# Performance work log

Hardware: AMD Instinct MI355X
Metric: run time of the kernel (lower is better)

The kernel has to match this reference:

```python
import jax, jax.numpy as jnp
import numpy as np

R = 64  # all tensor-ring ranks equal

def setup_inputs() -> dict:
    key = jax.random.key(0)
    k1, k2, k3 = jax.random.split(key, 3)
    B, T, N, M, C = 512, 64, 512, 64, 100
    # xavier-uniform-ish scale for weights (gain=init_value=1.0)
    s_sh = float(np.sqrt(6.0 / (R * N + R)))
    s_la = float(np.sqrt(6.0 / (C * R * M + R)))
    return {
        "tensor": jax.random.normal(k1, (B, T, N), dtype=jnp.float32),
        "W_shared": jax.random.uniform(k2, (R, N, R), dtype=jnp.float32, minval=-s_sh, maxval=s_sh),
        "W_last": jax.random.uniform(k3, (C, R, M, R), dtype=jnp.float32, minval=-s_la, maxval=s_la),
    }

def reference(tensor, W_shared, W_last):
    B = tensor.shape[0]
    xt = jnp.transpose(tensor, (1, 0, 2))  # [T, B, N]
    state0 = jnp.ones((R, B, R), dtype=tensor.dtype)  # [r1, B, r2]
    # per-step: x = einsum('bj,rbi->rbji'); state = einsum('ijk,rbji->rbk')
    # == einsum('bj,rbi,ijk->rbk'); factored to avoid the [r,b,n,r] intermediate
    def step(state, x_t):
        bik = jnp.einsum('bj,ijk->bik', x_t, W_shared)   # [B, r2, r3]
        new = jnp.einsum('rbi,bik->rbk', state, bik)     # [r1, B, r3]
        return new, None
    state, _ = jax.lax.scan(step, state0, xt)
    # last kernel with pad_input = ones(B, m):
    # einsum('cijk,rbji->cbrk') with x[r,b,j,i]=state[r,b,i] == sum over j of W_last
    W_sum = jnp.sum(W_last, axis=2)                      # [C, r2, r_last]
    state = jnp.einsum('cik,rbi->cbrk', W_sum, state)    # [C, B, r1, r_last]
    # trace over the last two (square) rank dims
    out = jnp.einsum('cbrr->cb', state)                  # [C, B]
    return out
```

## Files before the change

### kernel.cpp

```cpp
#include <hip/hip_runtime.h>
#include <hip/hip_fp16.h>


typedef _Float16 f16;
typedef __attribute__((ext_vector_type(8))) _Float16 f16x8;
typedef __attribute__((ext_vector_type(2))) _Float16 f16x2;
typedef __attribute__((ext_vector_type(4))) float f32x4;

#define GLDS16(g, l)                                                      \
    __builtin_amdgcn_global_load_lds(                                     \
        (const __attribute__((address_space(1))) void*)(g),               \
        (__attribute__((address_space(3))) void*)(l), 16, 0, 0)

#define BARRIER() asm volatile("s_barrier" ::: "memory")
#define VMCNT(n) asm volatile("s_waitcnt vmcnt(" #n ")" ::: "memory")

__global__ __launch_bounds__(256) void k_usum(const float* __restrict__ Wl,
                                              float* __restrict__ u) {
    int ci = blockIdx.x;
    const float4* p = (const float4*)(Wl + (size_t)ci * 4096);
    int tid = threadIdx.x;
    float s = 0.f;
#pragma unroll
    for (int q = 0; q < 4; ++q) {
        float4 v = p[tid + 256 * q];
        s += v.x + v.y + v.z + v.w;
    }
    __shared__ float red[256];
    red[tid] = s;
    __syncthreads();
    if (tid < 128) red[tid] += red[tid + 128];
    __syncthreads();
    if (tid < 64) {
        float x = red[tid] + red[tid + 64];
#pragma unroll
        for (int off = 32; off > 0; off >>= 1) x += __shfl_down(x, off, 64);
        if (tid == 0) u[ci] = x;
    }
}

__global__ __launch_bounds__(256) void k_cvtA(const float* __restrict__ in,
                                              f16* __restrict__ out) {
    int idx = blockIdx.x * 256 + threadIdx.x;
    const float4* p = (const float4*)in + (size_t)idx * 2;
    float4 v0 = p[0], v1 = p[1];
    f16x8 h;
    h[0] = (f16)v0.x; h[1] = (f16)v0.y; h[2] = (f16)v0.z; h[3] = (f16)v0.w;
    h[4] = (f16)v1.x; h[5] = (f16)v1.y; h[6] = (f16)v1.z; h[7] = (f16)v1.w;
    *(f16x8*)(out + (size_t)idx * 8) = h;
}

__global__ __launch_bounds__(256) void k_cvtW(const float* __restrict__ W,
                                              f16* __restrict__ Bt) {
    int o = blockIdx.x * 256 + threadIdx.x;
    int col = o >> 8;
    int j = (o & 255) << 1;
    int i = col >> 6, k = col & 63;
    const float* src = W + ((size_t)i * 512 + j) * 64 + k;
    f16x2 pk;
    pk[0] = (f16)src[0];
    pk[1] = (f16)src[64];
    *(f16x2*)(Bt + (size_t)col * 512 + j) = pk;
}


#define STAGE_A(qq, ha, ktv) do {                                             \
    _Pragma("unroll") for (int u_ = 0; u_ < 2; ++u_) {                        \
        int idx_ = (wid * 2 + u_) * 64 + lane;                                \
        int r_ = idx_ >> 3;                                                   \
        int ls_ = (idx_ & 7) ^ (r_ & 7);                                      \
        const f16* g_ = A + (size_t)(m0 + (ha) * 128 + r_) * 512              \
                          + (ktv) * 64 + ls_ * 8;                             \
        char* l_ = smem + (qq) * 65536 + (ha) * 16384 + (wid * 2 + u_) * 1024;\
        GLDS16(g_, l_);                                                       \
    } } while (0)

#define STAGE_B(qq, hb, ktv) do {                                             \
    _Pragma("unroll") for (int u_ = 0; u_ < 2; ++u_) {                        \
        int idx_ = (wid * 2 + u_) * 64 + lane;                                \
        int r_ = idx_ >> 3;                                                   \
        int ls_ = (idx_ & 7) ^ (r_ & 7);                                      \
        const f16* g_ = Bt + (size_t)(n0 + (hb) * 128 + r_) * 512             \
                           + (ktv) * 64 + ls_ * 8;                            \
        char* l_ = smem + (qq) * 65536 + 32768 + (hb) * 16384                 \
                        + (wid * 2 + u_) * 1024;                              \
        GLDS16(g_, l_);                                                       \
    } } while (0)

#define RD_A(ha, ktv) do {                                                    \
    _Pragma("unroll") for (int mf_ = 0; mf_ < 4; ++mf_)                       \
    _Pragma("unroll") for (int kq_ = 0; kq_ < 2; ++kq_) {                     \
        int ra_ = wr * 64 + mf_ * 16 + (lane & 15);                           \
        int off_ = ((ra_ << 7) + kq_ * 64 + ((lane >> 4) << 4))               \
                   ^ ((ra_ & 7) << 4);                                        \
        a[mf_][kq_] = *(const f16x8*)(smem + ((ktv) & 1) * 65536              \
                                      + (ha) * 16384 + off_);                 \
    } } while (0)

#define RD_B(hb, ktv, breg) do {                                              \
    _Pragma("unroll") for (int nf_ = 0; nf_ < 2; ++nf_)                       \
    _Pragma("unroll") for (int kq_ = 0; kq_ < 2; ++kq_) {                     \
        int rb_ = wc * 32 + nf_ * 16 + (lane & 15);                           \
        int off_ = ((rb_ << 7) + kq_ * 64 + ((lane >> 4) << 4))               \
                   ^ ((rb_ & 7) << 4);                                        \
        breg[nf_][kq_] = *(const f16x8*)(smem + ((ktv) & 1) * 65536           \
                                         + 32768 + (hb) * 16384 + off_);      \
    } } while (0)

#define MFMA_Q(qa_, qb_, breg) do {                                           \
    __builtin_amdgcn_s_setprio(1);                                            \
    _Pragma("unroll") for (int mf_ = 0; mf_ < 4; ++mf_)                       \
    _Pragma("unroll") for (int nf_ = 0; nf_ < 2; ++nf_)                       \
    _Pragma("unroll") for (int kq_ = 0; kq_ < 2; ++kq_)                       \
        acc[qa_][qb_][mf_][nf_] = __builtin_amdgcn_mfma_f32_16x16x32_f16(     \
            a[mf_][kq_], breg[nf_][kq_], acc[qa_][qb_][mf_][nf_], 0, 0, 0);   \
    __builtin_amdgcn_s_setprio(0);                                            \
    } while (0)

__global__ __launch_bounds__(512) void k_gemm_256(const f16* __restrict__ A,
                                                  const f16* __restrict__ Bt,
                                                  __half* __restrict__ outp) {
    extern __shared__ char smem[];
    const int tid = threadIdx.x;
    const int lane = tid & 63;
    const int wid = tid >> 6;
    int lin = blockIdx.x;
    int swz = (lin & 7) * 256 + (lin >> 3);
    const int n0 = (swz & 15) * 256;
    const int m0 = (swz >> 4) * 256;
    const int wr = wid >> 2, wc = wid & 3;

    f32x4 acc[2][2][4][2];
#pragma unroll
    for (int x = 0; x < 2; ++x)
#pragma unroll
        for (int y = 0; y < 2; ++y)
#pragma unroll
            for (int z = 0; z < 4; ++z)
#pragma unroll
                for (int w = 0; w < 2; ++w) acc[x][y][z][w] = (f32x4)0.f;

    f16x8 a[4][2], b0[2][2], b1[2][2];

    STAGE_A(0, 0, 0);
    STAGE_B(0, 0, 0);
    STAGE_B(0, 1, 0);
    STAGE_A(0, 1, 0);
    STAGE_A(1, 0, 1);
    STAGE_B(1, 0, 1);
    STAGE_B(1, 1, 1);

    for (int kt = 0; kt < 6; ++kt) {
        VMCNT(6);
        BARRIER();
        RD_A(0, kt);
        RD_B(0, kt, b0);
        STAGE_A((kt + 1) & 1, 1, kt + 1);
        MFMA_Q(0, 0, b0);
        BARRIER();
        RD_B(1, kt, b1);
        MFMA_Q(0, 1, b1);
        BARRIER();
        RD_A(1, kt);
        STAGE_A(kt & 1, 0, kt + 2);
        STAGE_B(kt & 1, 0, kt + 2);
        MFMA_Q(1, 0, b0);
        BARRIER();
        STAGE_B(kt & 1, 1, kt + 2);
        MFMA_Q(1, 1, b1);
        BARRIER();
    }
    {
        VMCNT(6);
        BARRIER();
        RD_A(0, 6);
        RD_B(0, 6, b0);
        STAGE_A(1, 1, 7);
        MFMA_Q(0, 0, b0);
        BARRIER();
        RD_B(1, 6, b1);
        MFMA_Q(0, 1, b1);
        BARRIER();
        RD_A(1, 6);
        MFMA_Q(1, 0, b0);
        BARRIER();
        MFMA_Q(1, 1, b1);
        BARRIER();
    }
    {
        VMCNT(0);
        BARRIER();
        RD_A(0, 7);
        RD_B(0, 7, b0);
        MFMA_Q(0, 0, b0);
        BARRIER();
        RD_B(1, 7, b1);
        MFMA_Q(0, 1, b1);
        BARRIER();
        RD_A(1, 7);
        MFMA_Q(1, 0, b0);
        BARRIER();
        MFMA_Q(1, 1, b1);
        BARRIER();
    }

    __half* Cs = (__half*)smem;
#pragma unroll
    for (int qa = 0; qa < 2; ++qa)
#pragma unroll
        for (int qb = 0; qb < 2; ++qb)
#pragma unroll
            for (int mf = 0; mf < 4; ++mf)
#pragma unroll
                for (int nf = 0; nf < 2; ++nf)
#pragma unroll
                    for (int j = 0; j < 4; ++j) {
                        int row = qa * 128 + wr * 64 + mf * 16 + ((lane >> 4) << 2) + j;
                        int col = qb * 128 + wc * 32 + nf * 16 + (lane & 15);
                        Cs[row * 256 + col] = __float2half(acc[qa][qb][mf][nf][j]);
                    }
    BARRIER();
#pragma unroll
    for (int it = 0; it < 16; ++it) {
        int idx = it * 512 + tid;
        int r = idx >> 5, seg = idx & 31;
        *(float4*)(outp + (size_t)(m0 + r) * 4096 + n0 + seg * 8) =
            *(const float4*)(Cs + r * 256 + seg * 8);
    }
}

#define BM 128
#define BN 64
#define BK 32
__global__ __launch_bounds__(256) void k_gemm(const float* __restrict__ A,
                                              const float* __restrict__ W,
                                              __half* __restrict__ out,
                                              int a_off, int a_stride) {
    __shared__ float As[BK * BM];
    __shared__ float Bs[BK * BN];
    int i0 = blockIdx.x;
    int m0 = blockIdx.y * BM;
    int tid = threadIdx.x;
    int tx = tid & 15, ty = tid >> 4;
    float acc[8][4];
#pragma unroll
    for (int q = 0; q < 8; ++q)
#pragma unroll
        for (int c = 0; c < 4; ++c) acc[q][c] = 0.f;
    const float* wbase = W + (size_t)i0 * 32768;
    for (int j0 = 0; j0 < 512; j0 += BK) {
        {
            int c4 = tid & 7;
            int r = tid >> 3;
#pragma unroll
            for (int p = 0; p < 4; ++p) {
                int row = r + 32 * p;
                float4 v = *(const float4*)(A + (size_t)a_off +
                                            (size_t)(m0 + row) * a_stride + j0 + 4 * c4);
                As[(4 * c4 + 0) * BM + row] = v.x;
                As[(4 * c4 + 1) * BM + row] = v.y;
                As[(4 * c4 + 2) * BM + row] = v.z;
                As[(4 * c4 + 3) * BM + row] = v.w;
            }
            const float4* src = (const float4*)(wbase + (size_t)j0 * 64);
            float4* dst = (float4*)Bs;
            dst[tid] = src[tid];
            dst[tid + 256] = src[tid + 256];
        }
        __syncthreads();
#pragma unroll
        for (int kk = 0; kk < BK; ++kk) {
            float bv[4], av[8];
#pragma unroll
            for (int c = 0; c < 4; ++c) bv[c] = Bs[kk * BN + 4 * tx + c];
#pragma unroll
            for (int q = 0; q < 8; ++q) av[q] = As[kk * BM + 8 * ty + q];
#pragma unroll
            for (int q = 0; q < 8; ++q)
#pragma unroll
                for (int c = 0; c < 4; ++c) acc[q][c] += av[q] * bv[c];
        }
        __syncthreads();
    }
#pragma unroll
    for (int q = 0; q < 8; ++q) {
        int m = m0 + 8 * ty + q;
        __half* o = out + (size_t)m * 4096 + i0 * 64 + 4 * tx;
#pragma unroll
        for (int c = 0; c < 4; ++c) o[c] = __float2half(acc[q][c]);
    }
}

__global__ __launch_bounds__(256) void k_scan(const __half* __restrict__ bik,
                                              const float* __restrict__ u,
                                              float* __restrict__ out) {
    int b = blockIdx.x;
    int tid = threadIdx.x;
    int k = tid & 63, grp = tid >> 6;
    __shared__ float vsh[64];
    __shared__ float part[256];
    if (tid < 64) vsh[tid] = 1.0f;
    const __half* base = bik + (size_t)b * 64 * 4096 + grp * 16 * 64 + k;
    __half bufA[16], bufB[16];
#pragma unroll
    for (int q = 0; q < 16; ++q) bufA[q] = base[q * 64];
    __syncthreads();
    for (int t = 0; t < 64; t += 2) {
        {
            const __half* pn = base + (size_t)(t + 1) * 4096;
#pragma unroll
            for (int q = 0; q < 16; ++q) bufB[q] = pn[q * 64];
            float s = 0.f;
#pragma unroll
            for (int q = 0; q < 16; ++q) s += vsh[grp * 16 + q] * __half2float(bufA[q]);
            part[tid] = s;
            __syncthreads();
            if (tid < 64) vsh[k] = part[k] + part[64 + k] + part[128 + k] + part[192 + k];
            __syncthreads();
        }
        {
            int t2 = (t + 2 < 64) ? (t + 2) : 63;
            const __half* pn = base + (size_t)t2 * 4096;
#pragma unroll
            for (int q = 0; q < 16; ++q) bufA[q] = pn[q * 64];
            float s = 0.f;
#pragma unroll
            for (int q = 0; q < 16; ++q) s += vsh[grp * 16 + q] * __half2float(bufB[q]);
            part[tid] = s;
            __syncthreads();
            if (tid < 64) vsh[k] = part[k] + part[64 + k] + part[128 + k] + part[192 + k];
            __syncthreads();
        }
    }
    if (tid < 100) {
        const float* uc = u + tid * 64;
        float s = 0.f;
#pragma unroll 8
        for (int i = 0; i < 64; ++i) s += uc[i] * vsh[i];
        out[tid * 512 + b] = s;
    }
}

__global__ __launch_bounds__(256) void k_update(const __half* __restrict__ Mt,
                                                const float* __restrict__ vin,
                                                float* __restrict__ vout, int first) {
    int o = blockIdx.x * 256 + threadIdx.x;
    int b = o >> 6, k = o & 63;
    const __half* m = Mt + (size_t)b * 4096;
    float s = 0.f;
    if (first) {
#pragma unroll 8
        for (int i = 0; i < 64; ++i) s += __half2float(m[i * 64 + k]);
    } else {
        const float* v = vin + (size_t)b * 64;
#pragma unroll 8
        for (int i = 0; i < 64; ++i) s += v[i] * __half2float(m[i * 64 + k]);
    }
    vout[o] = s;
}

__global__ __launch_bounds__(256) void k_final(const float* __restrict__ u,
                                               const float* __restrict__ v,
                                               float* __restrict__ out) {
    int o = blockIdx.x * 256 + threadIdx.x;
    int c = o >> 9, b = o & 511;
    const float* uc = u + c * 64;
    const float* vb = v + (size_t)b * 64;
    float s = 0.f;
#pragma unroll 8
    for (int i = 0; i < 64; ++i) s += uc[i] * vb[i];
    out[o] = s;
}

extern "C" void kernel_launch(void* const* d_in, const int* in_sizes, int n_in,
                              void* d_out, int out_size, void* d_ws, size_t ws_size,
                              hipStream_t stream) {
    const float* tensor = (const float*)d_in[0];
    const float* Wsh = (const float*)d_in[1];
    const float* Wl = (const float*)d_in[2];
    float* out = (float*)d_out;
    char* ws = (char*)d_ws;

    const size_t bik_bytes = (size_t)32768 * 4096 * sizeof(__half);
    const size_t fast_bytes = bik_bytes + (512u << 10) + ((size_t)16777216 * 2) + ((size_t)4096 * 512 * 2);

    if (ws_size >= fast_bytes) {
        __half* bik = (__half*)ws;
        float* u = (float*)(ws + bik_bytes);
        f16* Af16 = (f16*)(ws + bik_bytes + (512u << 10));
        f16* Btw = Af16 + (size_t)16777216;

        k_cvtA<<<8192, 256, 0, stream>>>(tensor, Af16);
        k_cvtW<<<4096, 256, 0, stream>>>(Wsh, Btw);
        k_usum<<<6400, 256, 0, stream>>>(Wl, u);
        (void)hipFuncSetAttribute((const void*)k_gemm_256,
                                  hipFuncAttributeMaxDynamicSharedMemorySize, 131072);
        k_gemm_256<<<2048, 512, 131072, stream>>>(Af16, Btw, bik);
        k_scan<<<512, 256, 0, stream>>>(bik, u, out);
    } else if (ws_size >= bik_bytes + (2u << 20)) {
        __half* bik = (__half*)ws;
        float* u = (float*)(ws + bik_bytes);

        k_usum<<<6400, 256, 0, stream>>>(Wl, u);
        dim3 g(64, 256);
        k_gemm<<<g, 256, 0, stream>>>(tensor, Wsh, bik, 0, 512);
        k_scan<<<512, 256, 0, stream>>>(bik, u, out);
    } else {
        __half* bikt = (__half*)ws;
        float* u = (float*)(ws + (size_t)(4 << 20));
        float* v0 = (float*)(ws + (size_t)(4 << 20) + (64 << 10));
        float* v1 = v0 + 32768;

        k_usum<<<6400, 256, 0, stream>>>(Wl, u);
        for (int t = 0; t < 64; ++t) {
            dim3 g(64, 4);
            k_gemm<<<g, 256, 0, stream>>>(tensor, Wsh, bikt, t * 512, 32768);
            float* vin = (t & 1) ? v0 : v1;
            float* vout = (t & 1) ? v1 : v0;
            k_update<<<128, 256, 0, stream>>>(bikt, (t == 0) ? v0 : vin, vout, t == 0);
        }
        k_final<<<200, 256, 0, stream>>>(u, v1, out);
    }
}
```

Before: 282.8 us.

## Fuse prep kernels, use nontemporal GEMM stores, LDS double-buffer scan loads

Merges the three preprocessing kernels (fp16 conversion of the input, transpose and convert of W_shared, W_last sum) into one launch dispatched by block index, which removes two launch gaps. The GEMM epilogue now writes bik with nontemporal stores so the large intermediate does not pollute the cache. The scan kernel now stages each 8 KB per-step matrix into LDS with double-buffered async global-to-LDS loads instead of strided per-thread half loads, aiming to coalesce memory traffic and overlap the load with compute. The cost is an extra vmcnt wait and barrier in every scan step.

Result: faster. 265.6 us (-6.1%).

```diff
diff --git a/kernel.cpp b/kernel.cpp
--- a/kernel.cpp
+++ b/kernel.cpp
@@ -39,28 +39,53 @@
     }
 }
 
-__global__ __launch_bounds__(256) void k_cvtA(const float* __restrict__ in,
-                                              f16* __restrict__ out) {
-    int idx = blockIdx.x * 256 + threadIdx.x;
-    const float4* p = (const float4*)in + (size_t)idx * 2;
-    float4 v0 = p[0], v1 = p[1];
-    f16x8 h;
-    h[0] = (f16)v0.x; h[1] = (f16)v0.y; h[2] = (f16)v0.z; h[3] = (f16)v0.w;
-    h[4] = (f16)v1.x; h[5] = (f16)v1.y; h[6] = (f16)v1.z; h[7] = (f16)v1.w;
-    *(f16x8*)(out + (size_t)idx * 8) = h;
-}
-
-__global__ __launch_bounds__(256) void k_cvtW(const float* __restrict__ W,
-                                              f16* __restrict__ Bt) {
-    int o = blockIdx.x * 256 + threadIdx.x;
-    int col = o >> 8;
-    int j = (o & 255) << 1;
-    int i = col >> 6, k = col & 63;
-    const float* src = W + ((size_t)i * 512 + j) * 64 + k;
-    f16x2 pk;
-    pk[0] = (f16)src[0];
-    pk[1] = (f16)src[64];
-    *(f16x2*)(Bt + (size_t)col * 512 + j) = pk;
+__global__ __launch_bounds__(256) void k_prep(const float* __restrict__ tensor,
+                                              const float* __restrict__ Wsh,
+                                              const float* __restrict__ Wl,
+                                              f16* __restrict__ Af16,
+                                              f16* __restrict__ Btw,
+                                              float* __restrict__ u) {
+    __shared__ float red[256];
+    int blk = blockIdx.x;
+    int tid = threadIdx.x;
+    if (blk < 8192) {
+        int idx = blk * 256 + tid;
+        const float4* p = (const float4*)tensor + (size_t)idx * 2;
+        float4 v0 = p[0], v1 = p[1];
+        f16x8 h;
+        h[0] = (f16)v0.x; h[1] = (f16)v0.y; h[2] = (f16)v0.z; h[3] = (f16)v0.w;
+        h[4] = (f16)v1.x; h[5] = (f16)v1.y; h[6] = (f16)v1.z; h[7] = (f16)v1.w;
+        *(f16x8*)(Af16 + (size_t)idx * 8) = h;
+    } else if (blk < 12288) {
+        int o = (blk - 8192) * 256 + tid;
+        int col = o >> 8;
+        int j = (o & 255) << 1;
+        int i = col >> 6, k = col & 63;
+        const float* src = Wsh + ((size_t)i * 512 + j) * 64 + k;
+        f16x2 pk;
+        pk[0] = (f16)src[0];
+        pk[1] = (f16)src[64];
+        *(f16x2*)(Btw + (size_t)col * 512 + j) = pk;
+    } else {
+        int ci = blk - 12288;
+        const float4* p = (const float4*)(Wl + (size_t)ci * 4096);
+        float s = 0.f;
+#pragma unroll
+        for (int q = 0; q < 4; ++q) {
+            float4 v = p[tid + 256 * q];
+            s += v.x + v.y + v.z + v.w;
+        }
+        red[tid] = s;
+        __syncthreads();
+        if (tid < 128) red[tid] += red[tid + 128];
+        __syncthreads();
+        if (tid < 64) {
+            float x = red[tid] + red[tid + 64];
+#pragma unroll
+            for (int off = 32; off > 0; off >>= 1) x += __shfl_down(x, off, 64);
+            if (tid == 0) u[ci] = x;
+        }
+    }
 }
 
 
@@ -224,8 +249,9 @@
     for (int it = 0; it < 16; ++it) {
         int idx = it * 512 + tid;
         int r = idx >> 5, seg = idx & 31;
-        *(float4*)(outp + (size_t)(m0 + r) * 4096 + n0 + seg * 8) =
-            *(const float4*)(Cs + r * 256 + seg * 8);
+        __builtin_nontemporal_store(
+            *(const f32x4*)(Cs + r * 256 + seg * 8),
+            (f32x4*)(outp + (size_t)(m0 + r) * 4096 + n0 + seg * 8));
     }
 }
 
@@ -294,43 +320,45 @@
 __global__ __launch_bounds__(256) void k_scan(const __half* __restrict__ bik,
                                               const float* __restrict__ u,
                                               float* __restrict__ out) {
+    __shared__ char sm[2][8192];
+    __shared__ float vsh[64];
+    __shared__ float part[256];
     int b = blockIdx.x;
     int tid = threadIdx.x;
     int k = tid & 63, grp = tid >> 6;
-    __shared__ float vsh[64];
-    __shared__ float part[256];
+    const int lane = tid & 63;
+    const int wid = tid >> 6;
     if (tid < 64) vsh[tid] = 1.0f;
-    const __half* base = bik + (size_t)b * 64 * 4096 + grp * 16 * 64 + k;
-    __half bufA[16], bufB[16];
-#pragma unroll
-    for (int q = 0; q < 16; ++q) bufA[q] = base[q * 64];
-    __syncthreads();
-    for (int t = 0; t < 64; t += 2) {
-        {
-            const __half* pn = base + (size_t)(t + 1) * 4096;
-#pragma unroll
-            for (int q = 0; q < 16; ++q) bufB[q] = pn[q * 64];
-            float s = 0.f;
-#pragma unroll
-            for (int q = 0; q < 16; ++q) s += vsh[grp * 16 + q] * __half2float(bufA[q]);
-            part[tid] = s;
-            __syncthreads();
-            if (tid < 64) vsh[k] = part[k] + part[64 + k] + part[128 + k] + part[192 + k];
-            __syncthreads();
-        }
-        {
-            int t2 = (t + 2 < 64) ? (t + 2) : 63;
-            const __half* pn = base + (size_t)t2 * 4096;
-#pragma unroll
-            for (int q = 0; q < 16; ++q) bufA[q] = pn[q * 64];
-            float s = 0.f;
-#pragma unroll
-            for (int q = 0; q < 16; ++q) s += vsh[grp * 16 + q] * __half2float(bufB[q]);
-            part[tid] = s;
-            __syncthreads();
-            if (tid < 64) vsh[k] = part[k] + part[64 + k] + part[128 + k] + part[192 + k];
-            __syncthreads();
-        }
+    const char* base = (const char*)(bik + (size_t)b * 64 * 4096);
+
+#pragma unroll
+    for (int u_ = 0; u_ < 2; ++u_) {
+        const char* g = base + (wid * 2 + u_) * 1024 + lane * 16;
+        GLDS16(g, &sm[0][0] + (wid * 2 + u_) * 1024);
+    }
+
+    for (int t = 0; t < 64; ++t) {
+        VMCNT(0);
+        __syncthreads();
+        if (t < 63) {
+            const char* gb = base + (size_t)(t + 1) * 8192;
+#pragma unroll
+            for (int u_ = 0; u_ < 2; ++u_) {
+                const char* g = gb + (wid * 2 + u_) * 1024 + lane * 16;
+                GLDS16(g, &sm[(t + 1) & 1][0] + (wid * 2 + u_) * 1024);
+            }
+        }
+        const __half* Mt = (const __half*)&sm[t & 1][0];
+        float s = 0.f;
+#pragma unroll
+        for (int q = 0; q < 16; ++q) {
+            int i = grp * 16 + q;
+            s += vsh[i] * __half2float(Mt[i * 64 + k]);
+        }
+        part[tid] = s;
+        __syncthreads();
+        if (tid < 64) vsh[k] = part[k] + part[64 + k] + part[128 + k] + part[192 + k];
+        __syncthreads();
     }
     if (tid < 100) {
         const float* uc = u + tid * 64;
@@ -390,9 +418,7 @@
         f16* Af16 = (f16*)(ws + bik_bytes + (512u << 10));
         f16* Btw = Af16 + (size_t)16777216;
 
-        k_cvtA<<<8192, 256, 0, stream>>>(tensor, Af16);
-        k_cvtW<<<4096, 256, 0, stream>>>(Wsh, Btw);
-        k_usum<<<6400, 256, 0, stream>>>(Wl, u);
+        k_prep<<<18688, 256, 0, stream>>>(tensor, Wsh, Wl, Af16, Btw, u);
         (void)hipFuncSetAttribute((const void*)k_gemm_256,
                                   hipFuncAttributeMaxDynamicSharedMemorySize, 131072);
         k_gemm_256<<<2048, 512, 131072, stream>>>(Af16, Btw, bik);
```
